# Kernel tuning notes

Measured on AMD Instinct MI355X. Metric: run time of the kernel, lower is better.

## Reference

```python
import jax, jax.numpy as jnp
import numpy as np

B, H, E, V = 128, 1024, 1024, 40000
L, S, A = 256, 10, 10
L_S, L_A = 1.0, 1.0  # s_copy_lambda / a_copy_lambda
NEG = -1e24


def setup_inputs():
    key = jax.random.key(0)
    ks = jax.random.split(key, 32)
    n = lambda i, shape: jax.random.normal(ks[i], shape, dtype=jnp.float32)
    p = lambda i, shape: jax.random.normal(ks[i], shape, dtype=jnp.float32) * 0.02
    rnn_in = 3 * E + H  # embed + history ctx (H) + state ctx (E) + action ctx (E)
    return {
        "inp": n(0, (B, 1, E)),
        "hidden": n(1, (1, B, H)),
        "hs_vectors": n(2, (B, L, H)),
        "state_gumbel_prob": jax.random.uniform(ks[3], (B, S, V), dtype=jnp.float32),
        "state_gumbel_embed": n(4, (B, S, E)),
        "action_gumbel_prob": jax.random.uniform(ks[5], (B, A, V), dtype=jnp.float32),
        "action_gumbel_embed": n(6, (B, A, E)),
        "history_lens": jax.random.randint(ks[7], (B,), 1, L + 1),
        "history_word_indices": jax.random.randint(ks[8], (B, L), 0, V),
        # history word mlp-attention
        "Wq_hist": p(9, (H, H)), "bq_hist": jnp.zeros((H,), jnp.float32),
        "Wm_hist": p(10, (H, H)), "v_hist": p(11, (H,)),
        # init_s_attn / init_a_attn (query H, memory E)
        "Wq_s": p(12, (H, H)), "bq_s": jnp.zeros((H,), jnp.float32),
        "Wm_s": p(13, (E, H)), "v_s": p(14, (H,)),
        "Wq_a": p(15, (H, H)), "bq_a": jnp.zeros((H,), jnp.float32),
        "Wm_a": p(16, (E, H)), "v_a": p(17, (H,)),
        # sparse_copy_attn (memory E+1)
        "Wq_sc": p(18, (H, H)), "bq_sc": jnp.zeros((H,), jnp.float32),
        "Wm_sc": p(19, (E + 1, H)), "v_sc": p(20, (H,)),
        # GRU (torch layout: [3H, in], gate order r,z,n)
        "W_ih": p(21, (3 * H, rnn_in)), "W_hh": p(22, (3 * H, H)),
        "b_ih": jnp.zeros((3 * H,), jnp.float32), "b_hh": jnp.zeros((3 * H,), jnp.float32),
        # output projection
        "W_out": p(23, (H, V)), "b_out": jnp.zeros((V,), jnp.float32),
    }


def _mlp_scores(q, mem, Wq, bq, Wm, v):
    # q: [B,1,H], mem: [B,L,M] -> additive-attention logits [B,1,L]
    t = jnp.tanh((q @ Wq + bq) + (mem @ Wm))  # [B,L,H]
    return (t @ v)[:, None, :]


def reference(inp, hidden, hs_vectors, state_gumbel_prob, state_gumbel_embed,
              action_gumbel_prob, action_gumbel_embed, history_lens,
              history_word_indices, Wq_hist, bq_hist, Wm_hist, v_hist,
              Wq_s, bq_s, Wm_s, v_s, Wq_a, bq_a, Wm_a, v_a,
              Wq_sc, bq_sc, Wm_sc, v_sc, W_ih, W_hh, b_ih, b_hh, W_out, b_out):
    q0 = jnp.transpose(hidden, (1, 0, 2))  # [B,1,H]
    # --- history word attention (masked mlp attention) ---
    hist_scores = _mlp_scores(q0, hs_vectors, Wq_hist, bq_hist, Wm_hist, v_hist)
    valid = jnp.arange(L)[None, None, :] < history_lens[:, None, None]
    hist_scores = jnp.where(valid, hist_scores, NEG)
    c_his = jax.nn.softmax(hist_scores, axis=-1) @ hs_vectors  # [B,1,H]
    # --- init_consult over state / action gumbel embeddings ---
    sw = jax.nn.softmax(_mlp_scores(q0, state_gumbel_embed, Wq_s, bq_s, Wm_s, v_s), axis=-1)
    c_state = sw @ state_gumbel_embed  # [B,1,E]
    aw = jax.nn.softmax(_mlp_scores(q0, action_gumbel_embed, Wq_a, bq_a, Wm_a, v_a), axis=-1)
    c_action = aw @ action_gumbel_embed  # [B,1,E]
    x = jnp.concatenate([inp, c_his, c_state, c_action], axis=-1)[:, 0, :]  # [B,3E+H]
    # --- single-step GRU cell (torch semantics, gate order r,z,n) ---
    h0 = hidden[0]
    gi = x @ W_ih.T + b_ih
    gh = h0 @ W_hh.T + b_hh
    ir, iz, inn = jnp.split(gi, 3, axis=-1)
    hr, hz, hn = jnp.split(gh, 3, axis=-1)
    r = jax.nn.sigmoid(ir + hr)
    z = jax.nn.sigmoid(iz + hz)
    nact = jnp.tanh(inn + r * hn)
    h_new = (1.0 - z) * nact + z * h0  # [B,H]
    # --- vocab logits + copy logits, joint softmax ---
    gene_logits = h_new @ W_out + b_out  # [B,V]
    cq = h_new[:, None, :]
    hs_logits = jnp.einsum('bqh,blh->bql', cq, hs_vectors)[:, 0, :]  # dot attn, [B,L]
    s_tag = jnp.zeros((B, S, 1), jnp.float32)
    a_tag = jnp.ones((B, A, 1), jnp.float32)
    st_logits = _mlp_scores(cq, jnp.concatenate([state_gumbel_embed, s_tag], -1), Wq_sc, bq_sc, Wm_sc, v_sc)[:, 0, :]
    ac_logits = _mlp_scores(cq, jnp.concatenate([action_gumbel_embed, a_tag], -1), Wq_sc, bq_sc, Wm_sc, v_sc)[:, 0, :]
    all_logits = jnp.concatenate([gene_logits, hs_logits, st_logits, ac_logits], axis=-1)
    wp = jax.nn.softmax(all_logits, axis=-1)  # [B, V+L+S+A]
    gene_p = wp[:, :V]
    hs_w = wp[:, V:V + L]
    st_w = wp[:, V + L:V + L + S]
    ac_w = wp[:, V + L + S:]
    # --- copy-distribution mixing ---
    scp = jnp.einsum('bs,bsv->bv', st_w, state_gumbel_prob)
    acp = jnp.einsum('ba,bav->bv', ac_w, action_gumbel_prob)
    gene_p = gene_p + L_S * scp + L_A * acp
    copy_p = jnp.zeros((B, V), jnp.float32).at[jnp.arange(B)[:, None], history_word_indices].add(hs_w)
    out = jnp.log(gene_p + copy_p)[:, None, :]  # [B,1,V]
    return out, h_new[None]
```

## Files before the change

### kernel.cpp

```cpp
#include <hip/hip_runtime.h>
#include <stdint.h>

typedef __attribute__((ext_vector_type(4))) float f32x4;
typedef __attribute__((ext_vector_type(2))) unsigned int u32x2;
typedef __attribute__((ext_vector_type(4))) unsigned int u32x4;
typedef __attribute__((ext_vector_type(8))) short bf16x8;

#define BV (128*40000)

__device__ __forceinline__ unsigned rne_bf16(float f) {
    unsigned x = __float_as_uint(f);
    return ((x + 0x7FFFu + ((x >> 16) & 1u)) >> 16) & 0xFFFFu;
}
__device__ __forceinline__ unsigned pack2(float a, float b) {
    return rne_bf16(a) | (rne_bf16(b) << 16);
}
__device__ __forceinline__ float bf2f(unsigned u) {
    return __uint_as_float((u & 0xFFFFu) << 16);
}
__device__ __forceinline__ float sigm(float x) { return 1.0f / (1.0f + expf(-x)); }
__device__ __forceinline__ float ftanh(float x) {
    float e = __expf(2.0f * x);
    return 1.0f - 2.0f / (e + 1.0f);
}

__device__ __forceinline__ void gload16(const void* g, void* l) {
    __builtin_amdgcn_global_load_lds(
        (const __attribute__((address_space(1))) unsigned*)g,
        (__attribute__((address_space(3))) unsigned*)l, 16, 0, 0);
}

__global__ __launch_bounds__(128) void k_prefix(
    const int* __restrict__ lens, int* __restrict__ prefix, int* __restrict__ nt) {
    __shared__ int sc[128];
    int t = threadIdx.x;
    sc[t] = lens[t];
    __syncthreads();
    for (int off = 1; off < 128; off <<= 1) {
        int x = (t >= off) ? sc[t - off] : 0;
        __syncthreads();
        sc[t] += x;
        __syncthreads();
    }
    if (t == 0) prefix[0] = 0;
    prefix[t + 1] = sc[t];
    if (t == 127) {
        int Mp = sc[127];
        nt[0] = 40 + (((Mp + 255) >> 8) << 2);
        nt[1] = Mp;
    }
}

struct BigArgs {
    const unsigned short *hs, *WmhT, *se, *ae, *WmsT, *WmaT;
    const float *qh_h, *bq_h, *v_h;
    const float *qh_s, *bq_s, *v_s;
    const float *qh_a, *bq_a, *v_a;
    float *hsc, *stsc, *acsc;
};

__global__ __launch_bounds__(512, 1) void k_big(
    BigArgs a, int* __restrict__ ctr, const int* __restrict__ prefix,
    const int* __restrict__ ntp) {
    __shared__ unsigned short As[2][16384];
    __shared__ unsigned short Bs[2][16384];
    __shared__ int sTile;
    __shared__ int rows_tab[256];

    const int nTiles = ntp[0], Mp = ntp[1];
    const int t = threadIdx.x, lane = t & 63, wv = t >> 6;
    const int l16 = lane & 15, lq = lane >> 4;
    const int wm = wv >> 2, wn = wv & 3;

    const int srowL = t >> 3;
    const int gccA = ((t & 7) ^ (srowL & 7)) << 3;
    const int sw = l16 & 7;
    const int c0 = ((lq ^ sw) << 3);
    const int A0 = (wm << 13) + (l16 << 6);
    const int B0 = ((wn >> 1) << 13) + ((((wn & 1) << 6) + l16) << 6);

#define STAGE(kt, d)                                                          \
    {                                                                         \
        _Pragma("unroll")                                                     \
        for (int q_ = 0; q_ < 4; ++q_) {                                      \
            int lo_ = (q_ << 12) + (wv << 9);                                 \
            gload16(gAr[q_] + (kt) * 64, &As[d][lo_]);                        \
            gload16(gB + (size_t)(q_ << 16) + (kt) * 64, &Bs[d][lo_]);        \
        }                                                                     \
    }

    for (;;) {
        __syncthreads();
        if (t == 0) sTile = atomicAdd(ctr, 1);
        __syncthreads();
        const int wg = sTile;
        if (wg >= nTiles) return;

        const unsigned short *Abase, *Bt;
        const float *rb, *cb, *vv;
        float* out;
        int m0, n0, vrows;
        bool hist;
        if (wg < 40) {
            hist = false;
            int op = wg / 20, r = wg - op * 20;
            int mt = r >> 2, nt2 = r & 3;
            if (op == 0) { Abase = a.se; Bt = a.WmsT; rb = a.qh_s; cb = a.bq_s; vv = a.v_s; out = a.stsc; }
            else         { Abase = a.ae; Bt = a.WmaT; rb = a.qh_a; cb = a.bq_a; vv = a.v_a; out = a.acsc; }
            m0 = mt << 8; n0 = nt2 << 8; vrows = 256;
        } else {
            hist = true;
            int h = wg - 40;
            int m = h >> 2, n = h & 3;
            Abase = a.hs; Bt = a.WmhT; rb = a.qh_h; cb = a.bq_h; vv = a.v_h; out = a.hsc;
            m0 = m << 8; n0 = n << 8;
            vrows = Mp - m0; if (vrows > 256) vrows = 256;
        }

        if (t < 256) {
            int rid;
            if (!hist) {
                rid = m0 + t;
            } else {
                int g = m0 + t;
                if (g < Mp) {
                    int lo = 0, hi = 128;
                    while (hi - lo > 1) {
                        int mid = (lo + hi) >> 1;
                        if (prefix[mid] <= g) lo = mid; else hi = mid;
                    }
                    rid = (lo << 8) + (g - prefix[lo]);
                } else {
                    rid = 0;
                }
            }
            rows_tab[t] = rid;
        }
        __syncthreads();

        const unsigned short* gAr[4];
#pragma unroll
        for (int q = 0; q < 4; ++q)
            gAr[q] = Abase + ((size_t)rows_tab[srowL + (q << 6)] << 10) + gccA;
        const unsigned short* gB = Bt + (size_t)(n0 + srowL) * 1024 + gccA;

        f32x4 acc[8][4];
#pragma unroll
        for (int i = 0; i < 8; ++i)
#pragma unroll
            for (int j = 0; j < 4; ++j) acc[i][j] = (f32x4){0.f, 0.f, 0.f, 0.f};

        STAGE(0, 0);
        for (int kt = 0; kt < 16; ++kt) {
            int cur = kt & 1;
            if (kt < 15) {
                STAGE(kt + 1, cur ^ 1);
                asm volatile("s_waitcnt vmcnt(8)" ::: "memory");
            } else {
                asm volatile("s_waitcnt vmcnt(0)" ::: "memory");
            }
            __builtin_amdgcn_s_barrier();
            __builtin_amdgcn_sched_barrier(0);

            const unsigned short* ab = As[cur];
            const unsigned short* bb = Bs[cur];
            if (vrows > (wm << 7)) {
                bf16x8 bf0[4], bf1[4];
#pragma unroll
                for (int nf = 0; nf < 4; ++nf) {
                    bf0[nf] = *(const bf16x8*)(bb + B0 + (nf << 10) + c0);
                    bf1[nf] = *(const bf16x8*)(bb + B0 + (nf << 10) + (c0 ^ 32));
                }
#pragma unroll
                for (int mf = 0; mf < 8; ++mf) {
                    if ((wm << 7) + (mf << 4) < vrows) {
                        bf16x8 a0 = *(const bf16x8*)(ab + A0 + (mf << 10) + c0);
                        bf16x8 a1 = *(const bf16x8*)(ab + A0 + (mf << 10) + (c0 ^ 32));
#pragma unroll
                        for (int nf = 0; nf < 4; ++nf)
                            acc[mf][nf] = __builtin_amdgcn_mfma_f32_16x16x32_bf16(a0, bf0[nf], acc[mf][nf], 0, 0, 0);
#pragma unroll
                        for (int nf = 0; nf < 4; ++nf)
                            acc[mf][nf] = __builtin_amdgcn_mfma_f32_16x16x32_bf16(a1, bf1[nf], acc[mf][nf], 0, 0, 0);
                    }
                }
            }
            __builtin_amdgcn_sched_barrier(0);
            __builtin_amdgcn_s_barrier();
        }

        float cbv[4], vvv[4];
        int gcs[4];
#pragma unroll
        for (int nf = 0; nf < 4; ++nf) {
            int gc = n0 + (wn << 6) + (nf << 4) + l16;
            gcs[nf] = gc; cbv[nf] = cb[gc]; vvv[nf] = vv[gc];
        }
#pragma unroll
        for (int mf = 0; mf < 8; ++mf) {
            int rloc = (wm << 7) + (mf << 4);
            if (rloc < vrows) {
#pragma unroll
                for (int r = 0; r < 4; ++r) {
                    int lrow = rloc + (lq << 2) + r;
                    if (lrow >= vrows) continue;
                    int gr = m0 + lrow;
                    int bidx = hist ? (rows_tab[lrow] >> 8) : (gr / 10);
                    const float* rbp = rb + ((size_t)bidx << 10);
                    float s = 0.f;
#pragma unroll
                    for (int nf = 0; nf < 4; ++nf) {
                        float x = acc[mf][nf][r] + rbp[gcs[nf]] + cbv[nf];
                        s += ftanh(x) * vvv[nf];
                    }
#pragma unroll
                    for (int m2 = 1; m2 < 16; m2 <<= 1) s += __shfl_xor(s, m2, 64);
                    if (l16 == 0) atomicAdd(&out[gr], s);
                }
            }
        }
    }
#undef STAGE
}

template<int EPI>
__device__ __forceinline__ void mgemm(
    const unsigned short* __restrict__ A, const unsigned short* __restrict__ Bt,
    float* __restrict__ out, const float* __restrict__ rb,
    const float* __restrict__ cb1, const float* __restrict__ cb2,
    const float* __restrict__ vvec,
    int m0, int n0, int kb, int ke, int ldk, int ldc, int rpb)
{
    __shared__ unsigned short As[2][4096];
    __shared__ unsigned short Bs[2][4096];
    const int t = threadIdx.x, lane = t & 63, wv = t >> 6;
    const int l16 = lane & 15, lq = lane >> 4;
    const int wm = wv >> 1, wn = wv & 1;

    const int srow = lane >> 2, scol = (lane & 3) << 3;
    const unsigned short* gA0 = A + (size_t)(m0 + (wv << 4) + srow) * ldk + kb + scol;
    const unsigned short* gA1 = gA0 + (size_t)64 * ldk;
    const unsigned short* gB0 = Bt + (size_t)(n0 + (wv << 4) + srow) * ldk + kb + scol;
    const unsigned short* gB1 = gB0 + (size_t)64 * ldk;
    unsigned short* lA0 = &As[0][wv << 9];
    unsigned short* lA1 = &As[0][(wv + 4) << 9];
    unsigned short* lB0 = &Bs[0][wv << 9];
// ... 20 lines not shown
        const unsigned short* bb = Bs[s & 1];
        bf16x8 af[4], bfv[4];
#pragma unroll
        for (int i = 0; i < 4; ++i)
            af[i] = *(const bf16x8*)(ab + (((wm << 6) + (i << 4) + l16) << 5) + (lq << 3));
#pragma unroll
        for (int i = 0; i < 4; ++i)
            bfv[i] = *(const bf16x8*)(bb + (((wn << 6) + (i << 4) + l16) << 5) + (lq << 3));
#pragma unroll
        for (int mf = 0; mf < 4; ++mf)
#pragma unroll
            for (int nf = 0; nf < 4; ++nf)
                acc[mf][nf] = __builtin_amdgcn_mfma_f32_16x16x32_bf16(af[mf], bfv[nf], acc[mf][nf], 0, 0, 0);
    }

    if (EPI == 1) {
#pragma unroll
        for (int mf = 0; mf < 4; ++mf) {
#pragma unroll
            for (int r = 0; r < 4; ++r) {
                int gr = m0 + (wm << 6) + (mf << 4) + (lq << 2) + r;
                const float* rbp = rb + (size_t)(gr / rpb) * 1024;
                float s = 0.0f;
#pragma unroll
                for (int nf = 0; nf < 4; ++nf) {
                    int gc = n0 + (wn << 6) + (nf << 4) + l16;
                    float xv = acc[mf][nf][r] + rbp[gc] + cb1[gc];
                    if (cb2) xv += cb2[gc];
                    s += ftanh(xv) * vvec[gc];
                }
#pragma unroll
                for (int msk = 1; msk < 16; msk <<= 1) s += __shfl_xor(s, msk, 64);
                if (l16 == 0) atomicAdd(&out[gr], s);
            }
        }
    } else {
#pragma unroll
        for (int mf = 0; mf < 4; ++mf) {
            int gr0 = m0 + (wm << 6) + (mf << 4) + (lq << 2);
#pragma unroll
            for (int nf = 0; nf < 4; ++nf) {
                int gc = n0 + (wn << 6) + (nf << 4) + l16;
#pragma unroll
                for (int r = 0; r < 4; ++r)
                    atomicAdd(&out[(size_t)(gr0 + r) * ldc + gc], acc[mf][nf][r]);
            }
        }
    }
}

__device__ __forceinline__ void gene_body(
    const unsigned short* __restrict__ hnb, const float* __restrict__ Wout,
    const float* __restrict__ b_out, float* __restrict__ out, int n0)
{
    __shared__ unsigned short As[2][4096];
    __shared__ unsigned short Bs[2][4096];
    const int t = threadIdx.x, lane = t & 63, wv = t >> 6;
    const int l16 = lane & 15, lq = lane >> 4;
    const int wm = wv >> 1, wn = wv & 1;

    const int srow = lane >> 2, scol = (lane & 3) << 3;
// ... 49 lines not shown
    for (int mf = 0; mf < 4; ++mf) {
        int gr0 = (wm << 6) + (mf << 4) + (lq << 2);
#pragma unroll
        for (int nf = 0; nf < 4; ++nf) {
            int gc = n0 + (wn << 6) + (nf << 4) + l16;
            if (gc < 40000) {
                float bo = b_out[gc];
#pragma unroll
                for (int r = 0; r < 4; ++r)
                    out[(size_t)(gr0 + r) * 40000 + gc] = acc[mf][nf][r] + bo;
            }
        }
    }
}

__global__ __launch_bounds__(256) void k_stac3(
    const unsigned short* se, const unsigned short* ae, const unsigned short* WmscT,
    const float* tagrow, const float* qsc, const float* bq_sc, const float* v_sc,
    float* stlg, float* aclg) {
    if (blockIdx.z == 0)
        mgemm<1>(se, WmscT, stlg, qsc, bq_sc, nullptr, v_sc, blockIdx.y * 128, blockIdx.x * 128, 0, 1024, 1024, 0, 10);
    else
        mgemm<1>(ae, WmscT, aclg, qsc, bq_sc, tagrow, v_sc, blockIdx.y * 128, blockIdx.x * 128, 0, 1024, 1024, 0, 10);
}

__global__ __launch_bounds__(256) void k_qh4(
    const unsigned short* q0, const unsigned short* W0, const unsigned short* W1,
    const unsigned short* W2, float* o0, float* o1, float* o2) {
    const unsigned short* W = W0; float* o = o0;
    if (blockIdx.z == 1) { W = W1; o = o1; }
    if (blockIdx.z == 2) { W = W2; o = o2; }
    int kb = blockIdx.y << 8;
    mgemm<2>(q0, W, o, nullptr, nullptr, nullptr, nullptr, 0, blockIdx.x * 128, kb, kb + 256, 1024, 1024, 1);
}

__global__ __launch_bounds__(256) void k_gigh2(
    const unsigned short* xb, const unsigned short* q0,
    const unsigned short* Wih, const unsigned short* Whh, float* gi, float* gh) {
    if (blockIdx.z == 0) {
        int kb = blockIdx.y << 9;
        mgemm<2>(xb, Wih, gi, nullptr, nullptr, nullptr, nullptr, 0, blockIdx.x * 128, kb, kb + 512, 4096, 3072, 1);
    } else {
        if (blockIdx.y >= 2) return;
        int kb = blockIdx.y << 9;
        mgemm<2>(q0, Whh, gh, nullptr, nullptr, nullptr, nullptr, 0, blockIdx.x * 128, kb, kb + 512, 1024, 3072, 1);
    }
}

__global__ __launch_bounds__(256) void k_qsc_gene(
    const unsigned short* hnb, const unsigned short* WqscT, float* qsc,
    const float* Wout, const float* b_out, float* out) {
    int id = blockIdx.x;
    if (id < 16) {
        int x = id & 7, kb = (id >> 3) << 9;
        mgemm<2>(hnb, WqscT, qsc, nullptr, nullptr, nullptr, nullptr, 0, x * 128, kb, kb + 512, 1024, 1024, 1);
    } else {
        gene_body(hnb, Wout, b_out, out, (id - 16) << 7);
    }
}

struct CvtArgs { const float* s[6]; unsigned short* d[6]; int pre[7]; };
__global__ __launch_bounds__(256) void k_cvt_all(CvtArgs a) {
    int total = a.pre[6];
    for (int i = blockIdx.x * 256 + threadIdx.x; i < total; i += gridDim.x * 256) {
        int seg = 0;
        while (i >= a.pre[seg + 1]) ++seg;
        int loc = i - a.pre[seg];
        const f32x4* s4 = (const f32x4*)a.s[seg] + (size_t)loc * 2;
        f32x4 q0 = s4[0], q1 = s4[1];
        ((u32x4*)a.d[seg])[loc] =
            (u32x4){pack2(q0[0],q0[1]), pack2(q0[2],q0[3]), pack2(q1[0],q1[1]), pack2(q1[2],q1[3])};
    }
}

struct TrArgs { const float* s[8]; unsigned short* d[8]; };
__global__ __launch_bounds__(256) void k_trcvt(TrArgs a) {
    __shared__ float tile[64][65];
    const float* in = a.s[blockIdx.z];
    unsigned short* ot = a.d[blockIdx.z];
    int k0 = blockIdx.y << 6, n0 = blockIdx.x << 6;
    int tr = threadIdx.x >> 6, tc = threadIdx.x & 63;
#pragma unroll
    for (int i = 0; i < 16; ++i) {
        int r = (i << 2) + tr;
        tile[r][tc] = in[(size_t)(k0 + r) * 1024 + n0 + tc];
    }
    __syncthreads();
#pragma unroll
    for (int i = 0; i < 16; ++i) {
        int r = (i << 2) + tr;
        ot[(size_t)(n0 + r) * 1024 + k0 + tc] = (unsigned short)rne_bf16(tile[tc][r]);
    }
}

__device__ __forceinline__ void softmax10(const float* src, float* dst) {
    float m = src[0];
    for (int i = 1; i < 10; ++i) m = fmaxf(m, src[i]);
    float z = 0.f, e[10];
    for (int i = 0; i < 10; ++i) { e[i] = expf(src[i] - m); z += e[i]; }
    float iz = 1.0f / z;
    for (int i = 0; i < 10; ++i) dst[i] = e[i] * iz;
}

__global__ __launch_bounds__(256) void k_ctx(
    const float* __restrict__ scores, const int* __restrict__ lens,
    const int* __restrict__ prefix,
// ... 43 lines not shown
        float ws = sw[q], wa = aw[q];
        cs0 += ws * bf2f(us[0]); cs1 += ws * bf2f(us[0] >> 16);
        cs2 += ws * bf2f(us[1]); cs3 += ws * bf2f(us[1] >> 16);
        ca0 += wa * bf2f(ua[0]); ca1 += wa * bf2f(ua[0] >> 16);
        ca2 += wa * bf2f(ua[1]); ca3 += wa * bf2f(ua[1] >> 16);
    }
    *((u32x2*)(xb + (size_t)b * 4096 + 2048) + t) = (u32x2){pack2(cs0, cs1), pack2(cs2, cs3)};
    *((u32x2*)(xb + (size_t)b * 4096 + 3072) + t) = (u32x2){pack2(ca0, ca1), pack2(ca2, ca3)};
}

__global__ __launch_bounds__(1024) void k_gruhsl(
    const float* __restrict__ gi, const float* __restrict__ gh,
    const float* __restrict__ b_ih, const float* __restrict__ b_hh,
    const float* __restrict__ h0, float* __restrict__ hnew,
    unsigned short* __restrict__ hnb,
    const unsigned short* __restrict__ hs, float* __restrict__ hsl) {
    int b = blockIdx.x, y = blockIdx.y, j = threadIdx.x;
    size_t i = (size_t)b * 1024 + j;
    const float* gib = gi + (size_t)b * 3072;
    const float* ghb = gh + (size_t)b * 3072;
    float r = sigm(gib[j] + b_ih[j] + ghb[j] + b_hh[j]);
    float z = sigm(gib[1024 + j] + b_ih[1024 + j] + ghb[1024 + j] + b_hh[1024 + j]);
    float hn = ghb[2048 + j] + b_hh[2048 + j];
    float n = tanhf(gib[2048 + j] + b_ih[2048 + j] + r * hn);
    float h = (1.0f - z) * n + z * h0[i];
    if (y == 0) {
        hnew[i] = h;
        hnb[i] = (unsigned short)rne_bf16(h);
    }
    __shared__ float hsm[1024];
    hsm[j] = h;
    __syncthreads();
    int wave = j >> 6, lane = j & 63;
    float hr[16];
#pragma unroll
    for (int k = 0; k < 16; ++k) hr[k] = hsm[lane * 16 + k];
    for (int l = (y << 7) + wave; l < (y << 7) + 128; l += 16) {
        const u32x4* row = (const u32x4*)(hs + ((size_t)b * 256 + l) * 1024);
        u32x4 u0 = row[lane * 2], u1 = row[lane * 2 + 1];
        float s = hr[0]*bf2f(u0[0]) + hr[1]*bf2f(u0[0]>>16) + hr[2]*bf2f(u0[1]) + hr[3]*bf2f(u0[1]>>16)
                + hr[4]*bf2f(u0[2]) + hr[5]*bf2f(u0[2]>>16) + hr[6]*bf2f(u0[3]) + hr[7]*bf2f(u0[3]>>16)
                + hr[8]*bf2f(u1[0]) + hr[9]*bf2f(u1[0]>>16) + hr[10]*bf2f(u1[1]) + hr[11]*bf2f(u1[1]>>16)
                + hr[12]*bf2f(u1[2]) + hr[13]*bf2f(u1[2]>>16) + hr[14]*bf2f(u1[3]) + hr[15]*bf2f(u1[3]>>16);
#pragma unroll
        for (int msk = 1; msk < 64; msk <<= 1) s += __shfl_xor(s, msk, 64);
        if (lane == 0) hsl[b * 256 + l] = s;
    }
}

__global__ __launch_bounds__(256) void k_smsc(
    const float* __restrict__ gene, const float* __restrict__ hsl,
    const float* __restrict__ stl, const float* __restrict__ acl,
    const int* __restrict__ hwi,
    float* __restrict__ mbuf, float* __restrict__ zbuf, float* __restrict__ copyp) {
    int b = blockIdx.x, t = threadIdx.x;
    __shared__ float red[256];
    const f32x4* g4 = (const f32x4*)(gene + (size_t)b * 40000);
    float mx = -3.0e38f;
    for (int i = t; i < 10000; i += 256) {
        f32x4 q = g4[i];
        mx = fmaxf(mx, fmaxf(fmaxf(q[0], q[1]), fmaxf(q[2], q[3])));
    }
    float hv = hsl[b * 256 + t];
    mx = fmaxf(mx, hv);
    if (t < 10) mx = fmaxf(mx, fmaxf(stl[b * 10 + t], acl[b * 10 + t]));
    red[t] = mx; __syncthreads();
    for (int s = 128; s > 0; s >>= 1) { if (t < s) red[t] = fmaxf(red[t], red[t + s]); __syncthreads(); }
    float m = red[0];
    __syncthreads();
    float sum = 0.f;
    for (int i = t; i < 10000; i += 256) {
        f32x4 q = g4[i];
        sum += expf(q[0]-m) + expf(q[1]-m) + expf(q[2]-m) + expf(q[3]-m);
    }
    sum += expf(hv - m);
    if (t < 10) sum += expf(stl[b * 10 + t] - m) + expf(acl[b * 10 + t] - m);
    red[t] = sum; __syncthreads();
    for (int s = 128; s > 0; s >>= 1) { if (t < s) red[t] += red[t + s]; __syncthreads(); }
    float Z = red[0];
    if (t == 0) { mbuf[b] = m; zbuf[b] = Z; }
    float wv = expf(hv - m) / Z;
    atomicAdd(copyp + (size_t)b * 40000 + hwi[b * 256 + t], wv);
}

__global__ __launch_bounds__(256) void k_final(
    float* __restrict__ gene_out, const float* __restrict__ copyp,
    const float* __restrict__ sprob, const float* __restrict__ aprob,
    const float* __restrict__ stl, const float* __restrict__ acl,
    const float* __restrict__ mbuf, const float* __restrict__ zbuf) {
    int b = blockIdx.y, t = threadIdx.x;
    __shared__ float sw[10], aw[10];
// ... 48 lines not shown
#define SO_SE     33554432
#define SO_AE     34865152
#define SO_Q0     36175872
#define SO_X      36306944
#define SO_HNB    36831232
#define SO_WQHT   36962304
#define SO_WQST   38010880
#define SO_WQAT   39059456
#define SO_WQSCT  40108032
#define SO_WMHT   41156608
#define SO_WMST   42205184
#define SO_WMAT   43253760
#define SO_WMSCT  44302336
#define SO_WIH    45350912
#define SO_WHH    57933824

extern "C" void kernel_launch(void* const* d_in, const int* in_sizes, int n_in,
                              void* d_out, int out_size, void* d_ws, size_t ws_size,
                              hipStream_t stream) {
    const float* inp     = (const float*)d_in[0];
    const float* hidden  = (const float*)d_in[1];
    const float* hs      = (const float*)d_in[2];
    const float* sprob   = (const float*)d_in[3];
    const float* se      = (const float*)d_in[4];
    const float* aprob   = (const float*)d_in[5];
    const float* ae      = (const float*)d_in[6];
    const int*   lens    = (const int*)d_in[7];
    const int*   hwi     = (const int*)d_in[8];
    const float* Wq_hist = (const float*)d_in[9];
    const float* bq_hist = (const float*)d_in[10];
// ... 29 lines not shown
    float* stlg = w + OFF_STLG;  float* aclg = w + OFF_ACLG;
    float* hsl  = w + OFF_HSL;   float* mbuf = w + OFF_M;     float* zbuf = w + OFF_Z;
    float* copyp = w + OFF_COPY;
    int*   ctr  = (int*)(w + OFF_CTR);
    int*   pfx  = (int*)(w + OFF_PFX);
    int*   ntb  = (int*)(w + OFF_NT);

    unsigned short* hs_bf = sb + SO_HS;   unsigned short* se_bf = sb + SO_SE;
    unsigned short* ae_bf = sb + SO_AE;   unsigned short* q0_bf = sb + SO_Q0;
    unsigned short* x_bf  = sb + SO_X;    unsigned short* hnb   = sb + SO_HNB;
    unsigned short* WqhT  = sb + SO_WQHT; unsigned short* WqsT  = sb + SO_WQST;
    unsigned short* WqaT  = sb + SO_WQAT; unsigned short* WqscT = sb + SO_WQSCT;
    unsigned short* WmhT  = sb + SO_WMHT; unsigned short* WmsT  = sb + SO_WMST;
    unsigned short* WmaT  = sb + SO_WMAT; unsigned short* WmscT = sb + SO_WMSCT;
    unsigned short* WihB  = sb + SO_WIH;  unsigned short* WhhB  = sb + SO_WHH;

    dim3 blk(256);

    hipMemsetAsync(w, 0, (size_t)ZERO_FLOATS * 4, stream);
    hipMemsetAsync(copyp, 0, (size_t)BV * 4, stream);

    k_prefix<<<dim3(1), dim3(128), 0, stream>>>(lens, pfx, ntb);

    CvtArgs ca;
    ca.s[0]=hs; ca.s[1]=se; ca.s[2]=ae; ca.s[3]=hidden; ca.s[4]=W_ih; ca.s[5]=W_hh;
    ca.d[0]=hs_bf; ca.d[1]=se_bf; ca.d[2]=ae_bf; ca.d[3]=q0_bf; ca.d[4]=WihB; ca.d[5]=WhhB;
    ca.pre[0]=0; ca.pre[1]=4194304; ca.pre[2]=4358144; ca.pre[3]=4521984;
    ca.pre[4]=4538368; ca.pre[5]=6111232; ca.pre[6]=6504448;
    k_cvt_all<<<dim3(4096), blk, 0, stream>>>(ca);

    TrArgs ta;
    ta.s[0]=Wq_hist; ta.s[1]=Wq_s; ta.s[2]=Wq_a; ta.s[3]=Wq_sc;
    ta.s[4]=Wm_hist; ta.s[5]=Wm_s; ta.s[6]=Wm_a; ta.s[7]=Wm_sc;
    ta.d[0]=WqhT; ta.d[1]=WqsT; ta.d[2]=WqaT; ta.d[3]=WqscT;
    ta.d[4]=WmhT; ta.d[5]=WmsT; ta.d[6]=WmaT; ta.d[7]=WmscT;
    k_trcvt<<<dim3(16, 16, 8), blk, 0, stream>>>(ta);

    k_qh4<<<dim3(8, 4, 3), blk, 0, stream>>>(q0_bf, WqhT, WqsT, WqaT, qh_h, qh_s, qh_a);

    BigArgs ba;
    ba.hs = hs_bf; ba.WmhT = WmhT; ba.se = se_bf; ba.ae = ae_bf;
    ba.WmsT = WmsT; ba.WmaT = WmaT;
    ba.qh_h = qh_h; ba.bq_h = bq_hist; ba.v_h = v_hist;
    ba.qh_s = qh_s; ba.bq_s = bq_s; ba.v_s = v_s;
    ba.qh_a = qh_a; ba.bq_a = bq_a; ba.v_a = v_a;
    ba.hsc = hsc; ba.stsc = stsc; ba.acsc = acsc;
    k_big<<<dim3(256), dim3(512), 0, stream>>>(ba, ctr, pfx, ntb);

    k_ctx<<<dim3(128), blk, 0, stream>>>(hsc, lens, pfx, hs_bf, inp, stsc, acsc, se_bf, ae_bf, x_bf);
    k_gigh2<<<dim3(24, 8, 2), blk, 0, stream>>>(x_bf, q0_bf, WihB, WhhB, gi, gh);
    k_gruhsl<<<dim3(128, 2), dim3(1024), 0, stream>>>(gi, gh, b_ih, b_hh, hidden, hnew, hnb, hs_bf, hsl);
    k_qsc_gene<<<dim3(329), blk, 0, stream>>>(hnb, WqscT, qsc, W_out, b_out, out);
    k_stac3<<<dim3(8, 10, 2), blk, 0, stream>>>(se_bf, ae_bf, WmscT, Wm_sc + (size_t)1024 * 1024,
                                                qsc, bq_sc, v_sc, stlg, aclg);
    k_smsc<<<dim3(128), blk, 0, stream>>>(out, hsl, stlg, aclg, hwi, mbuf, zbuf, copyp);
    k_final<<<dim3(40, 128), blk, 0, stream>>>(out, copyp, sprob, aprob, stlg, aclg, mbuf, zbuf);

    (void)in_sizes; (void)n_in; (void)out_size; (void)ws_size;
}
```

Baseline: 556.5 us.

## Precompute copy-attention memory projections in big GEMM and fuse prep kernels

Moves the state/action memory projections through Wm_sc, which do not depend on h_new, into the persistent k_big GEMM as extra tiles stored in bf16. The later sparse-copy score becomes an elementwise tanh reduction inside the softmax kernel. The qsc projection is computed per row inside the GRU kernel, and the prefix, convert and transpose kernels are merged into one prep launch. The k_big main loop is also rewritten with interleaved partial staging and s_setprio scheduling. This cuts launches and removes the GEMM that sat on the critical path after the GRU. In exchange it adds GEMM work to k_big, rounds intermediates to bf16, and drops the per-row valid-rows guard inside the MFMA loop.

```diff
diff --git a/kernel.cpp b/kernel.cpp
--- a/kernel.cpp
+++ b/kernel.cpp
@@ -30,33 +30,13 @@
         (__attribute__((address_space(3))) unsigned*)l, 16, 0, 0);
 }
 
-__global__ __launch_bounds__(128) void k_prefix(
-    const int* __restrict__ lens, int* __restrict__ prefix, int* __restrict__ nt) {
-    __shared__ int sc[128];
-    int t = threadIdx.x;
-    sc[t] = lens[t];
-    __syncthreads();
-    for (int off = 1; off < 128; off <<= 1) {
-        int x = (t >= off) ? sc[t - off] : 0;
-        __syncthreads();
-        sc[t] += x;
-        __syncthreads();
-    }
-    if (t == 0) prefix[0] = 0;
-    prefix[t + 1] = sc[t];
-    if (t == 127) {
-        int Mp = sc[127];
-        nt[0] = 40 + (((Mp + 255) >> 8) << 2);
-        nt[1] = Mp;
-    }
-}
-
 struct BigArgs {
-    const unsigned short *hs, *WmhT, *se, *ae, *WmsT, *WmaT;
+    const unsigned short *hs, *WmhT, *se, *ae, *WmsT, *WmaT, *WmscT;
     const float *qh_h, *bq_h, *v_h;
     const float *qh_s, *bq_s, *v_s;
     const float *qh_a, *bq_a, *v_a;
     float *hsc, *stsc, *acsc;
+    unsigned short *mseh, *maeh;
 };
 
 __global__ __launch_bounds__(512, 1) void k_big(
@@ -71,23 +51,15 @@
     const int t = threadIdx.x, lane = t & 63, wv = t >> 6;
     const int l16 = lane & 15, lq = lane >> 4;
     const int wm = wv >> 2, wn = wv & 3;
-
     const int srowL = t >> 3;
     const int gccA = ((t & 7) ^ (srowL & 7)) << 3;
-    const int sw = l16 & 7;
-    const int c0 = ((lq ^ sw) << 3);
+    const int swz = l16 & 7;
+    const int c0 = ((lq ^ swz) << 3);
     const int A0 = (wm << 13) + (l16 << 6);
     const int B0 = ((wn >> 1) << 13) + ((((wn & 1) << 6) + l16) << 6);
 
-#define STAGE(kt, d)                                                          \
-    {                                                                         \
-        _Pragma("unroll")                                                     \
-        for (int q_ = 0; q_ < 4; ++q_) {                                      \
-            int lo_ = (q_ << 12) + (wv << 9);                                 \
-            gload16(gAr[q_] + (kt) * 64, &As[d][lo_]);                        \
-            gload16(gB + (size_t)(q_ << 16) + (kt) * 64, &Bs[d][lo_]);        \
-        }                                                                     \
-    }
+#define STQA(ktt, d, q) gload16(gAr[q] + (ktt) * 64, &As[d][((q) << 12) + (wv << 9)])
+#define STQB(ktt, d, q) gload16(gB + ((size_t)(q) << 16) + (ktt) * 64, &Bs[d][((q) << 12) + (wv << 9)])
 
     for (;;) {
         __syncthreads();
@@ -97,20 +69,28 @@
         if (wg >= nTiles) return;
 
         const unsigned short *Abase, *Bt;
-        const float *rb, *cb, *vv;
-        float* out;
-        int m0, n0, vrows;
-        bool hist;
+        const float *rb = nullptr, *cb = nullptr, *vv = nullptr;
+        float* out = nullptr;
+        unsigned short* outh = nullptr;
+        int m0, n0, vrows, cls;
         if (wg < 40) {
-            hist = false;
+            cls = 0;
             int op = wg / 20, r = wg - op * 20;
             int mt = r >> 2, nt2 = r & 3;
             if (op == 0) { Abase = a.se; Bt = a.WmsT; rb = a.qh_s; cb = a.bq_s; vv = a.v_s; out = a.stsc; }
             else         { Abase = a.ae; Bt = a.WmaT; rb = a.qh_a; cb = a.bq_a; vv = a.v_a; out = a.acsc; }
             m0 = mt << 8; n0 = nt2 << 8; vrows = 256;
+        } else if (wg < 80) {
+            cls = 1;
+            int r = wg - 40;
+            int op = r / 20; r -= op * 20;
+            int mt = r >> 2, nt2 = r & 3;
+            Abase = op ? a.ae : a.se; Bt = a.WmscT;
+            outh = op ? a.maeh : a.mseh;
+            m0 = mt << 8; n0 = nt2 << 8; vrows = 256;
         } else {
-            hist = true;
-            int h = wg - 40;
+            cls = 2;
+            int h = wg - 80;
             int m = h >> 2, n = h & 3;
             Abase = a.hs; Bt = a.WmhT; rb = a.qh_h; cb = a.bq_h; vv = a.v_h; out = a.hsc;
             m0 = m << 8; n0 = n << 8;
@@ -119,7 +99,7 @@
 
         if (t < 256) {
             int rid;
-            if (!hist) {
+            if (cls != 2) {
                 rid = m0 + t;
             } else {
                 int g = m0 + t;
@@ -150,86 +130,132 @@
 #pragma unroll
             for (int j = 0; j < 4; ++j) acc[i][j] = (f32x4){0.f, 0.f, 0.f, 0.f};
 
-        STAGE(0, 0);
+        STQA(0, 0, 0); STQA(0, 0, 2);
+        STQB(0, 0, 0); STQB(0, 0, 1); STQB(0, 0, 2); STQB(0, 0, 3);
+        STQA(0, 0, 1); STQA(0, 0, 3);
+        __builtin_amdgcn_sched_barrier(0);
+        asm volatile("s_waitcnt vmcnt(2)" ::: "memory");
+        __builtin_amdgcn_s_barrier();
+        __builtin_amdgcn_sched_barrier(0);
+
         for (int kt = 0; kt < 16; ++kt) {
-            int cur = kt & 1;
-            if (kt < 15) {
-                STAGE(kt + 1, cur ^ 1);
-                asm volatile("s_waitcnt vmcnt(8)" ::: "memory");
-            } else {
-                asm volatile("s_waitcnt vmcnt(0)" ::: "memory");
-            }
+            const int cur = kt & 1, dn = cur ^ 1, kn = kt + 1;
+            const bool pre = kt < 15;
+            const unsigned short* ab = As[cur];
+            const unsigned short* bb = Bs[cur];
+            bf16x8 bk0[4], bk1[4], af[4];
+            if (pre) { STQA(kn, dn, 0); STQA(kn, dn, 2); }
+#pragma unroll
+            for (int nf = 0; nf < 4; ++nf) bk0[nf] = *(const bf16x8*)(bb + B0 + (nf << 10) + c0);
+#pragma unroll
+            for (int mf = 0; mf < 4; ++mf) af[mf] = *(const bf16x8*)(ab + A0 + (mf << 10) + c0);
+            __builtin_amdgcn_s_setprio(1);
+#pragma unroll
+            for (int mf = 0; mf < 4; ++mf)
+#pragma unroll
+                for (int nf = 0; nf < 4; ++nf)
+                    acc[mf][nf] = __builtin_amdgcn_mfma_f32_16x16x32_bf16(af[mf], bk0[nf], acc[mf][nf], 0, 0, 0);
+            __builtin_amdgcn_s_setprio(0);
+            if (pre) { STQB(kn, dn, 0); STQB(kn, dn, 1); }
+#pragma unroll
+            for (int nf = 0; nf < 4; ++nf) bk1[nf] = *(const bf16x8*)(bb + B0 + (nf << 10) + (c0 ^ 32));
+#pragma unroll
+            for (int mf = 0; mf < 4; ++mf) af[mf] = *(const bf16x8*)(ab + A0 + (mf << 10) + (c0 ^ 32));
+            __builtin_amdgcn_s_setprio(1);
+#pragma unroll
+            for (int mf = 0; mf < 4; ++mf)
+#pragma unroll
+                for (int nf = 0; nf < 4; ++nf)
+                    acc[mf][nf] = __builtin_amdgcn_mfma_f32_16x16x32_bf16(af[mf], bk1[nf], acc[mf][nf], 0, 0, 0);
+            __builtin_amdgcn_s_setprio(0);
+            if (pre) { STQB(kn, dn, 2); STQB(kn, dn, 3); }
+            __builtin_amdgcn_sched_barrier(0);
+            if (pre) asm volatile("s_waitcnt vmcnt(6)" ::: "memory");
+            else     asm volatile("s_waitcnt vmcnt(0)" ::: "memory");
             __builtin_amdgcn_s_barrier();
             __builtin_amdgcn_sched_barrier(0);
-
-            const unsigned short* ab = As[cur];
-            const unsigned short* bb = Bs[cur];
-            if (vrows > (wm << 7)) {
-                bf16x8 bf0[4], bf1[4];
-#pragma unroll
-                for (int nf = 0; nf < 4; ++nf) {
-                    bf0[nf] = *(const bf16x8*)(bb + B0 + (nf << 10) + c0);
-                    bf1[nf] = *(const bf16x8*)(bb + B0 + (nf << 10) + (c0 ^ 32));
+#pragma unroll
+            for (int mf = 0; mf < 4; ++mf) af[mf] = *(const bf16x8*)(ab + A0 + ((4 + mf) << 10) + c0);
+            __builtin_amdgcn_s_setprio(1);
+#pragma unroll
+            for (int mf = 0; mf < 4; ++mf)
+#pragma unroll
+                for (int nf = 0; nf < 4; ++nf)
+                    acc[4 + mf][nf] = __builtin_amdgcn_mfma_f32_16x16x32_bf16(af[mf], bk0[nf], acc[4 + mf][nf], 0, 0, 0);
+            __builtin_amdgcn_s_setprio(0);
+            if (pre) { STQA(kn, dn, 1); STQA(kn, dn, 3); }
+#pragma unroll
+            for (int mf = 0; mf < 4; ++mf) af[mf] = *(const bf16x8*)(ab + A0 + ((4 + mf) << 10) + (c0 ^ 32));
+            __builtin_amdgcn_s_setprio(1);
+#pragma unroll
+            for (int mf = 0; mf < 4; ++mf)
+#pragma unroll
+                for (int nf = 0; nf < 4; ++nf)
+                    acc[4 + mf][nf] = __builtin_amdgcn_mfma_f32_16x16x32_bf16(af[mf], bk1[nf], acc[4 + mf][nf], 0, 0, 0);
+            __builtin_amdgcn_s_setprio(0);
+            __builtin_amdgcn_sched_barrier(0);
+            if (pre) asm volatile("s_waitcnt vmcnt(2)" ::: "memory");
+            else     asm volatile("s_waitcnt vmcnt(0)" ::: "memory");
+            __builtin_amdgcn_s_barrier();
+            __builtin_amdgcn_sched_barrier(0);
+        }
+
+        if (cls == 1) {
+            int gcs4[4];
+#pragma unroll
+            for (int nf = 0; nf < 4; ++nf) gcs4[nf] = n0 + (wn << 6) + (nf << 4) + l16;
+#pragma unroll
+            for (int mf = 0; mf < 8; ++mf) {
+#pragma unroll
+                for (int r = 0; r < 4; ++r) {
+                    int grow = m0 + (wm << 7) + (mf << 4) + (lq << 2) + r;
+#pragma unroll
+                    for (int nf = 0; nf < 4; ++nf)
+                        outh[(size_t)grow * 1024 + gcs4[nf]] = (unsigned short)rne_bf16(acc[mf][nf][r]);
                 }
-#pragma unroll
-                for (int mf = 0; mf < 8; ++mf) {
-                    if ((wm << 7) + (mf << 4) < vrows) {
-                        bf16x8 a0 = *(const bf16x8*)(ab + A0 + (mf << 10) + c0);
-                        bf16x8 a1 = *(const bf16x8*)(ab + A0 + (mf << 10) + (c0 ^ 32));
-#pragma unroll
-                        for (int nf = 0; nf < 4; ++nf)
-                            acc[mf][nf] = __builtin_amdgcn_mfma_f32_16x16x32_bf16(a0, bf0[nf], acc[mf][nf], 0, 0, 0);
-#pragma unroll
-                        for (int nf = 0; nf < 4; ++nf)
-                            acc[mf][nf] = __builtin_amdgcn_mfma_f32_16x16x32_bf16(a1, bf1[nf], acc[mf][nf], 0, 0, 0);
+            }
+        } else {
+            float cbv[4], vvv[4];
+            int gcs[4];
+#pragma unroll
+            for (int nf = 0; nf < 4; ++nf) {
+                int gc = n0 + (wn << 6) + (nf << 4) + l16;
+                gcs[nf] = gc; cbv[nf] = cb[gc]; vvv[nf] = vv[gc];
+            }
+#pragma unroll
+            for (int mf = 0; mf < 8; ++mf) {
+                int rloc = (wm << 7) + (mf << 4);
+                if (rloc < vrows) {
+#pragma unroll
+                    for (int r = 0; r < 4; ++r) {
+                        int lrow = rloc + (lq << 2) + r;
+                        if (lrow >= vrows) continue;
+                        int gr = m0 + lrow;
+                        int bidx = (cls == 2) ? (rows_tab[lrow] >> 8) : (gr / 10);
+                        const float* rbp = rb + ((size_t)bidx << 10);
+                        float s = 0.f;
+#pragma unroll
+                        for (int nf = 0; nf < 4; ++nf) {
+                            float x = acc[mf][nf][r] + rbp[gcs[nf]] + cbv[nf];
+                            s += ftanh(x) * vvv[nf];
+                        }
+#pragma unroll
+                        for (int m2 = 1; m2 < 16; m2 <<= 1) s += __shfl_xor(s, m2, 64);
+                        if (l16 == 0) atomicAdd(&out[gr], s);
                     }
                 }
             }
-            __builtin_amdgcn_sched_barrier(0);
-            __builtin_amdgcn_s_barrier();
-        }
-
-        float cbv[4], vvv[4];
-        int gcs[4];
-#pragma unroll
-        for (int nf = 0; nf < 4; ++nf) {
-            int gc = n0 + (wn << 6) + (nf << 4) + l16;
-            gcs[nf] = gc; cbv[nf] = cb[gc]; vvv[nf] = vv[gc];
-        }
-#pragma unroll
-        for (int mf = 0; mf < 8; ++mf) {
-            int rloc = (wm << 7) + (mf << 4);
-            if (rloc < vrows) {
-#pragma unroll
-                for (int r = 0; r < 4; ++r) {
-                    int lrow = rloc + (lq << 2) + r;
-                    if (lrow >= vrows) continue;
-                    int gr = m0 + lrow;
-                    int bidx = hist ? (rows_tab[lrow] >> 8) : (gr / 10);
-                    const float* rbp = rb + ((size_t)bidx << 10);
-                    float s = 0.f;
-#pragma unroll
-                    for (int nf = 0; nf < 4; ++nf) {
-                        float x = acc[mf][nf][r] + rbp[gcs[nf]] + cbv[nf];
-                        s += ftanh(x) * vvv[nf];
-                    }
-#pragma unroll
-                    for (int m2 = 1; m2 < 16; m2 <<= 1) s += __shfl_xor(s, m2, 64);
-                    if (l16 == 0) atomicAdd(&out[gr], s);
-                }
-            }
-        }
-    }
-#undef STAGE
+        }
+    }
+#undef STQA
+#undef STQB
 }
 
 template<int EPI>
 __device__ __forceinline__ void mgemm(
     const unsigned short* __restrict__ A, const unsigned short* __restrict__ Bt,
-    float* __restrict__ out, const float* __restrict__ rb,
-    const float* __restrict__ cb1, const float* __restrict__ cb2,
-    const float* __restrict__ vvec,
-    int m0, int n0, int kb, int ke, int ldk, int ldc, int rpb)
+    float* __restrict__ out,
+    int m0, int n0, int kb, int ke, int ldk, int ldc)
 {
     __shared__ unsigned short As[2][4096];
     __shared__ unsigned short Bs[2][4096];
@@ -280,37 +306,15 @@
                 acc[mf][nf] = __builtin_amdgcn_mfma_f32_16x16x32_bf16(af[mf], bfv[nf], acc[mf][nf], 0, 0, 0);
     }
 
-    if (EPI == 1) {
-#pragma unroll
-        for (int mf = 0; mf < 4; ++mf) {
-#pragma unroll
-            for (int r = 0; r < 4; ++r) {
-                int gr = m0 + (wm << 6) + (mf << 4) + (lq << 2) + r;
-                const float* rbp = rb + (size_t)(gr / rpb) * 1024;
-                float s = 0.0f;
-#pragma unroll
-                for (int nf = 0; nf < 4; ++nf) {
-                    int gc = n0 + (wn << 6) + (nf << 4) + l16;
-                    float xv = acc[mf][nf][r] + rbp[gc] + cb1[gc];
-                    if (cb2) xv += cb2[gc];
-                    s += ftanh(xv) * vvec[gc];
-                }
-#pragma unroll
-                for (int msk = 1; msk < 16; msk <<= 1) s += __shfl_xor(s, msk, 64);
-                if (l16 == 0) atomicAdd(&out[gr], s);
-            }
-        }
-    } else {
-#pragma unroll
-        for (int mf = 0; mf < 4; ++mf) {
-            int gr0 = m0 + (wm << 6) + (mf << 4) + (lq << 2);
-#pragma unroll
-            for (int nf = 0; nf < 4; ++nf) {
-                int gc = n0 + (wn << 6) + (nf << 4) + l16;
-#pragma unroll
-                for (int r = 0; r < 4; ++r)
-                    atomicAdd(&out[(size_t)(gr0 + r) * ldc + gc], acc[mf][nf][r]);
-            }
+#pragma unroll
+    for (int mf = 0; mf < 4; ++mf) {
+        int gr0 = m0 + (wm << 6) + (mf << 4) + (lq << 2);
+#pragma unroll
+        for (int nf = 0; nf < 4; ++nf) {
+            int gc = n0 + (wn << 6) + (nf << 4) + l16;
+#pragma unroll
+            for (int r = 0; r < 4; ++r)
+                atomicAdd(&out[(size_t)(gr0 + r) * ldc + gc], acc[mf][nf][r]);
         }
     }
 }
@@ -390,16 +394,6 @@
     }
 }
 
-__global__ __launch_bounds__(256) void k_stac3(
-    const unsigned short* se, const unsigned short* ae, const unsigned short* WmscT,
-    const float* tagrow, const float* qsc, const float* bq_sc, const float* v_sc,
-    float* stlg, float* aclg) {
-    if (blockIdx.z == 0)
-        mgemm<1>(se, WmscT, stlg, qsc, bq_sc, nullptr, v_sc, blockIdx.y * 128, blockIdx.x * 128, 0, 1024, 1024, 0, 10);
-    else
-        mgemm<1>(ae, WmscT, aclg, qsc, bq_sc, tagrow, v_sc, blockIdx.y * 128, blockIdx.x * 128, 0, 1024, 1024, 0, 10);
-}
-
 __global__ __launch_bounds__(256) void k_qh4(
     const unsigned short* q0, const unsigned short* W0, const unsigned short* W1,
     const unsigned short* W2, float* o0, float* o1, float* o2) {
@@ -407,7 +401,7 @@
     if (blockIdx.z == 1) { W = W1; o = o1; }
     if (blockIdx.z == 2) { W = W2; o = o2; }
     int kb = blockIdx.y << 8;
-    mgemm<2>(q0, W, o, nullptr, nullptr, nullptr, nullptr, 0, blockIdx.x * 128, kb, kb + 256, 1024, 1024, 1);
+    mgemm<2>(q0, W, o, 0, blockIdx.x * 128, kb, kb + 256, 1024, 1024);
 }
 
 __global__ __launch_bounds__(256) void k_gigh2(
@@ -415,57 +409,72 @@
     const unsigned short* Wih, const unsigned short* Whh, float* gi, float* gh) {
     if (blockIdx.z == 0) {
         int kb = blockIdx.y << 9;
-        mgemm<2>(xb, Wih, gi, nullptr, nullptr, nullptr, nullptr, 0, blockIdx.x * 128, kb, kb + 512, 4096, 3072, 1);
+        mgemm<2>(xb, Wih, gi, 0, blockIdx.x * 128, kb, kb + 512, 4096, 3072);
     } else {
         if (blockIdx.y >= 2) return;
         int kb = blockIdx.y << 9;
-        mgemm<2>(q0, Whh, gh, nullptr, nullptr, nullptr, nullptr, 0, blockIdx.x * 128, kb, kb + 512, 1024, 3072, 1);
-    }
-}
-
-__global__ __launch_bounds__(256) void k_qsc_gene(
-    const unsigned short* hnb, const unsigned short* WqscT, float* qsc,
-    const float* Wout, const float* b_out, float* out) {
-    int id = blockIdx.x;
-    if (id < 16) {
-        int x = id & 7, kb = (id >> 3) << 9;
-        mgemm<2>(hnb, WqscT, qsc, nullptr, nullptr, nullptr, nullptr, 0, x * 128, kb, kb + 512, 1024, 1024, 1);
+        mgemm<2>(q0, Whh, gh, 0, blockIdx.x * 128, kb, kb + 512, 1024, 3072);
+    }
+}
+
+__global__ __launch_bounds__(256) void k_gene(
+    const unsigned short* hnb, const float* Wout, const float* b_out, float* out) {
+    gene_body(hnb, Wout, b_out, out, (int)blockIdx.x << 7);
+}
+
+struct PrepArgs {
+    const float* cs[6]; unsigned short* cd[6]; int pre[7];
+    const float* ts[8]; unsigned short* td[8];
+    const int* lens; int* prefix; int* nt;
+};
+__global__ __launch_bounds__(256) void k_prep(PrepArgs a) {
+    int bid = blockIdx.x, t = threadIdx.x;
+    if (bid < 2048) {
+        __shared__ float tile[64][65];
+        int z = bid >> 8, rem = bid & 255, y = rem >> 4, x = rem & 15;
+        const float* in = a.ts[z];
+        unsigned short* ot = a.td[z];
+        int k0 = y << 6, n0 = x << 6;
+        int tr = t >> 6, tc = t & 63;
+#pragma unroll
+        for (int i = 0; i < 16; ++i) {
+            int r = (i << 2) + tr;
+            tile[r][tc] = in[(size_t)(k0 + r) * 1024 + n0 + tc];
+        }
+        __syncthreads();
+#pragma unroll
+        for (int i = 0; i < 16; ++i) {
+            int r = (i << 2) + tr;
+            ot[(size_t)(n0 + r) * 1024 + k0 + tc] = (unsigned short)rne_bf16(tile[tc][r]);
+        }
+    } else if (bid == 2048) {
+        __shared__ int sc[128];
+        if (t < 128) sc[t] = a.lens[t];
+        __syncthreads();
+        for (int off = 1; off < 128; off <<= 1) {
+            int x = (t >= off && t < 128) ? sc[t - off] : 0;
+            __syncthreads();
+            if (t < 128) sc[t] += x;
+            __syncthreads();
+        }
+        if (t == 0) a.prefix[0] = 0;
+        if (t < 128) a.prefix[t + 1] = sc[t];
+        if (t == 127) {
+            int Mp = sc[127];
+            a.nt[0] = 80 + (((Mp + 255) >> 8) << 2);
+            a.nt[1] = Mp;
+        }
     } else {
-        gene_body(hnb, Wout, b_out, out, (id - 16) << 7);
-    }
-}
-
-struct CvtArgs { const float* s[6]; unsigned short* d[6]; int pre[7]; };
-__global__ __launch_bounds__(256) void k_cvt_all(CvtArgs a) {
-    int total = a.pre[6];
-    for (int i = blockIdx.x * 256 + threadIdx.x; i < total; i += gridDim.x * 256) {
-        int seg = 0;
-        while (i >= a.pre[seg + 1]) ++seg;
-        int loc = i - a.pre[seg];
-        const f32x4* s4 = (const f32x4*)a.s[seg] + (size_t)loc * 2;
-        f32x4 q0 = s4[0], q1 = s4[1];
-        ((u32x4*)a.d[seg])[loc] =
-            (u32x4){pack2(q0[0],q0[1]), pack2(q0[2],q0[3]), pack2(q1[0],q1[1]), pack2(q1[2],q1[3])};
-    }
-}
-
-struct TrArgs { const float* s[8]; unsigned short* d[8]; };
-__global__ __launch_bounds__(256) void k_trcvt(TrArgs a) {
-    __shared__ float tile[64][65];
-    const float* in = a.s[blockIdx.z];
-    unsigned short* ot = a.d[blockIdx.z];
-    int k0 = blockIdx.y << 6, n0 = blockIdx.x << 6;
-    int tr = threadIdx.x >> 6, tc = threadIdx.x & 63;
-#pragma unroll
-    for (int i = 0; i < 16; ++i) {
-        int r = (i << 2) + tr;
-        tile[r][tc] = in[(size_t)(k0 + r) * 1024 + n0 + tc];
-    }
-    __syncthreads();
-#pragma unroll
-    for (int i = 0; i < 16; ++i) {
-        int r = (i << 2) + tr;
-        ot[(size_t)(n0 + r) * 1024 + k0 + tc] = (unsigned short)rne_bf16(tile[tc][r]);
+        int total = a.pre[6];
+        for (int i = (bid - 2049) * 256 + t; i < total; i += 2048 * 256) {
+            int seg = 0;
+            while (i >= a.pre[seg + 1]) ++seg;
+            int loc = i - a.pre[seg];
+            const f32x4* s4 = (const f32x4*)a.cs[seg] + (size_t)loc * 2;
+            f32x4 q0 = s4[0], q1 = s4[1];
+            ((u32x4*)a.cd[seg])[loc] =
+                (u32x4){pack2(q0[0],q0[1]), pack2(q0[2],q0[3]), pack2(q1[0],q1[1]), pack2(q1[2],q1[3])};
+        }
     }
 }
 
@@ -539,7 +548,8 @@
     const float* __restrict__ b_ih, const float* __restrict__ b_hh,
     const float* __restrict__ h0, float* __restrict__ hnew,
     unsigned short* __restrict__ hnb,
-    const unsigned short* __restrict__ hs, float* __restrict__ hsl) {
+    const unsigned short* __restrict__ hs, float* __restrict__ hsl,
+    const unsigned short* __restrict__ WqscT, float* __restrict__ qsc) {
     int b = blockIdx.x, y = blockIdx.y, j = threadIdx.x;
     size_t i = (size_t)b * 1024 + j;
     const float* gib = gi + (size_t)b * 3072;
@@ -556,6 +566,20 @@
     __shared__ float hsm[1024];
     hsm[j] = h;
     __syncthreads();
+    if (y == 0) {
+        float acn = 0.f;
+        const u32x4* wr = (const u32x4*)(WqscT + ((size_t)j << 10));
+#pragma unroll 4
+        for (int k8 = 0; k8 < 128; ++k8) {
+            u32x4 u = wr[k8];
+            const float* hp = hsm + (k8 << 3);
+            acn += hp[0]*bf2f(u[0]) + hp[1]*bf2f(u[0]>>16)
+                 + hp[2]*bf2f(u[1]) + hp[3]*bf2f(u[1]>>16)
+                 + hp[4]*bf2f(u[2]) + hp[5]*bf2f(u[2]>>16)
+                 + hp[6]*bf2f(u[3]) + hp[7]*bf2f(u[3]>>16);
+        }
+        qsc[(size_t)b * 1024 + j] = acn;
+    }
     int wave = j >> 6, lane = j & 63;
     float hr[16];
 #pragma unroll
@@ -575,11 +599,39 @@
 
 __global__ __launch_bounds__(256) void k_smsc(
     const float* __restrict__ gene, const float* __restrict__ hsl,
-    const float* __restrict__ stl, const float* __restrict__ acl,
-    const int* __restrict__ hwi,
+    const unsigned short* __restrict__ mseh, const unsigned short* __restrict__ maeh,
+    const float* __restrict__ qsc, const float* __restrict__ bq_sc,
+    const float* __restrict__ v_sc, const float* __restrict__ tagrow,
+    const int* __restrict__ hwi, float* __restrict__ stlg, float* __restrict__ aclg,
     float* __restrict__ mbuf, float* __restrict__ zbuf, float* __restrict__ copyp) {
     int b = blockIdx.x, t = threadIdx.x;
     __shared__ float red[256];
+    __shared__ float sst[10], sac[10];
+    const float* qb = qsc + (size_t)b * 1024;
+    for (int s = 0; s < 10; ++s) {
+        float ps = 0.f, pa = 0.f;
+        const unsigned short* ms = mseh + ((size_t)b * 10 + s) * 1024;
+        const unsigned short* ma = maeh + ((size_t)b * 10 + s) * 1024;
+#pragma unroll
+        for (int k = 0; k < 4; ++k) {
+            int c = t + (k << 8);
+            float qv = qb[c] + bq_sc[c];
+            float vc = v_sc[c];
+            ps += ftanh(bf2f(ms[c]) + qv) * vc;
+            pa += ftanh(bf2f(ma[c]) + qv + tagrow[c]) * vc;
+        }
+#pragma unroll
+        for (int msk = 1; msk < 64; msk <<= 1) { ps += __shfl_xor(ps, msk, 64); pa += __shfl_xor(pa, msk, 64); }
+        if ((t & 63) == 0) { red[t >> 6] = ps; red[4 + (t >> 6)] = pa; }
+        __syncthreads();
+        if (t == 0) {
+            float vs = red[0] + red[1] + red[2] + red[3];
+            float va = red[4] + red[5] + red[6] + red[7];
+            sst[s] = vs; sac[s] = va;
+            stlg[b * 10 + s] = vs; aclg[b * 10 + s] = va;
+        }
+        __syncthreads();
+    }
     const f32x4* g4 = (const f32x4*)(gene + (size_t)b * 40000);
     float mx = -3.0e38f;
     for (int i = t; i < 10000; i += 256) {
@@ -588,7 +640,7 @@
     }
     float hv = hsl[b * 256 + t];
     mx = fmaxf(mx, hv);
-    if (t < 10) mx = fmaxf(mx, fmaxf(stl[b * 10 + t], acl[b * 10 + t]));
+    if (t < 10) mx = fmaxf(mx, fmaxf(sst[t], sac[t]));
     red[t] = mx; __syncthreads();
     for (int s = 128; s > 0; s >>= 1) { if (t < s) red[t] = fmaxf(red[t], red[t + s]); __syncthreads(); }
     float m = red[0];
@@ -599,7 +651,7 @@
         sum += expf(q[0]-m) + expf(q[1]-m) + expf(q[2]-m) + expf(q[3]-m);
     }
     sum += expf(hv - m);
-    if (t < 10) sum += expf(stl[b * 10 + t] - m) + expf(acl[b * 10 + t] - m);
+    if (t < 10) sum += expf(sst[t] - m) + expf(sac[t] - m);
     red[t] = sum; __syncthreads();
     for (int s = 128; s > 0; s >>= 1) { if (t < s) red[t] += red[t + s]; __syncthreads(); }
     float Z = red[0];
@@ -678,6 +730,8 @@
 #define SO_WMSCT  44302336
 #define SO_WIH    45350912
 #define SO_WHH    57933824
+#define SO_MSE    61079552
+#define SO_MAE    62390272
 
 extern "C" void kernel_launch(void* const* d_in, const int* in_sizes, int n_in,
                               void* d_out, int out_size, void* d_ws, size_t ws_size,
@@ -737,46 +791,45 @@
     unsigned short* WmhT  = sb + SO_WMHT; unsigned short* WmsT  = sb + SO_WMST;
     unsigned short* WmaT  = sb + SO_WMAT; unsigned short* WmscT = sb + SO_WMSCT;
     unsigned short* WihB  = sb + SO_WIH;  unsigned short* WhhB  = sb + SO_WHH;
+    unsigned short* mseh  = sb + SO_MSE;  unsigned short* maeh  = sb + SO_MAE;
 
     dim3 blk(256);
 
     hipMemsetAsync(w, 0, (size_t)ZERO_FLOATS * 4, stream);
     hipMemsetAsync(copyp, 0, (size_t)BV * 4, stream);
 
-    k_prefix<<<dim3(1), dim3(128), 0, stream>>>(lens, pfx, ntb);
-
-    CvtArgs ca;
-    ca.s[0]=hs; ca.s[1]=se; ca.s[2]=ae; ca.s[3]=hidden; ca.s[4]=W_ih; ca.s[5]=W_hh;
-    ca.d[0]=hs_bf; ca.d[1]=se_bf; ca.d[2]=ae_bf; ca.d[3]=q0_bf; ca.d[4]=WihB; ca.d[5]=WhhB;
-    ca.pre[0]=0; ca.pre[1]=4194304; ca.pre[2]=4358144; ca.pre[3]=4521984;
-    ca.pre[4]=4538368; ca.pre[5]=6111232; ca.pre[6]=6504448;
-    k_cvt_all<<<dim3(4096), blk, 0, stream>>>(ca);
-
-    TrArgs ta;
-    ta.s[0]=Wq_hist; ta.s[1]=Wq_s; ta.s[2]=Wq_a; ta.s[3]=Wq_sc;
-    ta.s[4]=Wm_hist; ta.s[5]=Wm_s; ta.s[6]=Wm_a; ta.s[7]=Wm_sc;
-    ta.d[0]=WqhT; ta.d[1]=WqsT; ta.d[2]=WqaT; ta.d[3]=WqscT;
-    ta.d[4]=WmhT; ta.d[5]=WmsT; ta.d[6]=WmaT; ta.d[7]=WmscT;
-    k_trcvt<<<dim3(16, 16, 8), blk, 0, stream>>>(ta);
+    PrepArgs pa;
+    pa.cs[0]=hs; pa.cs[1]=se; pa.cs[2]=ae; pa.cs[3]=hidden; pa.cs[4]=W_ih; pa.cs[5]=W_hh;
+    pa.cd[0]=hs_bf; pa.cd[1]=se_bf; pa.cd[2]=ae_bf; pa.cd[3]=q0_bf; pa.cd[4]=WihB; pa.cd[5]=WhhB;
+    pa.pre[0]=0; pa.pre[1]=4194304; pa.pre[2]=4358144; pa.pre[3]=4521984;
+    pa.pre[4]=4538368; pa.pre[5]=6111232; pa.pre[6]=6504448;
+    pa.ts[0]=Wq_hist; pa.ts[1]=Wq_s; pa.ts[2]=Wq_a; pa.ts[3]=Wq_sc;
+    pa.ts[4]=Wm_hist; pa.ts[5]=Wm_s; pa.ts[6]=Wm_a; pa.ts[7]=Wm_sc;
+    pa.td[0]=WqhT; pa.td[1]=WqsT; pa.td[2]=WqaT; pa.td[3]=WqscT;
+    pa.td[4]=WmhT; pa.td[5]=WmsT; pa.td[6]=WmaT; pa.td[7]=WmscT;
+    pa.lens = lens; pa.prefix = pfx; pa.nt = ntb;
+    k_prep<<<dim3(4097), blk, 0, stream>>>(pa);
 
     k_qh4<<<dim3(8, 4, 3), blk, 0, stream>>>(q0_bf, WqhT, WqsT, WqaT, qh_h, qh_s, qh_a);
 
     BigArgs ba;
     ba.hs = hs_bf; ba.WmhT = WmhT; ba.se = se_bf; ba.ae = ae_bf;
-    ba.WmsT = WmsT; ba.WmaT = WmaT;
+    ba.WmsT = WmsT; ba.WmaT = WmaT; ba.WmscT = WmscT;
     ba.qh_h = qh_h; ba.bq_h = bq_hist; ba.v_h = v_hist;
     ba.qh_s = qh_s; ba.bq_s = bq_s; ba.v_s = v_s;
     ba.qh_a = qh_a; ba.bq_a = bq_a; ba.v_a = v_a;
     ba.hsc = hsc; ba.stsc = stsc; ba.acsc = acsc;
+    ba.mseh = mseh; ba.maeh = maeh;
     k_big<<<dim3(256), dim3(512), 0, stream>>>(ba, ctr, pfx, ntb);
 
     k_ctx<<<dim3(128), blk, 0, stream>>>(hsc, lens, pfx, hs_bf, inp, stsc, acsc, se_bf, ae_bf, x_bf);
     k_gigh2<<<dim3(24, 8, 2), blk, 0, stream>>>(x_bf, q0_bf, WihB, WhhB, gi, gh);
-    k_gruhsl<<<dim3(128, 2), dim3(1024), 0, stream>>>(gi, gh, b_ih, b_hh, hidden, hnew, hnb, hs_bf, hsl);
-    k_qsc_gene<<<dim3(329), blk, 0, stream>>>(hnb, WqscT, qsc, W_out, b_out, out);
-    k_stac3<<<dim3(8, 10, 2), blk, 0, stream>>>(se_bf, ae_bf, WmscT, Wm_sc + (size_t)1024 * 1024,
-                                                qsc, bq_sc, v_sc, stlg, aclg);
-    k_smsc<<<dim3(128), blk, 0, stream>>>(out, hsl, stlg, aclg, hwi, mbuf, zbuf, copyp);
+    k_gruhsl<<<dim3(128, 2), dim3(1024), 0, stream>>>(gi, gh, b_ih, b_hh, hidden, hnew, hnb,
+                                                      hs_bf, hsl, WqscT, qsc);
+    k_gene<<<dim3(313), blk, 0, stream>>>(hnb, W_out, b_out, out);
+    k_smsc<<<dim3(128), blk, 0, stream>>>(out, hsl, mseh, maeh, qsc, bq_sc, v_sc,
+                                          Wm_sc + (size_t)1024 * 1024, hwi, stlg, aclg,
+                                          mbuf, zbuf, copyp);
     k_final<<<dim3(40, 128), blk, 0, stream>>>(out, copyp, sprob, aprob, stlg, aclg, mbuf, zbuf);
 
     (void)in_sizes; (void)n_in; (void)out_size; (void)ws_size;
```

Result: slower. 580.8 us (+4.4%).
